# Kernel tuning notes

Measured on AMD Instinct MI355X. Metric: run time of the kernel, lower is better.

Reference implementation:

```python
import jax, jax.numpy as jnp
import numpy as np

SEQ_LEN = 720
PRED_LEN = 720
RANK = 16
CTX_DIM = 128
HID = 64
BATCH = 256


def setup_inputs() -> dict:
    key = jax.random.key(0)
    ks = jax.random.split(key, 8)
    x = jax.random.normal(ks[0], (BATCH, SEQ_LEN, 1), dtype=jnp.float32)
    ctx = jax.random.normal(ks[1], (BATCH, CTX_DIM), dtype=jnp.float32)
    # Base weight, xavier-uniform init
    limit = np.sqrt(6.0 / (PRED_LEN + SEQ_LEN)).astype(np.float32)
    W = jax.random.uniform(ks[2], (PRED_LEN, SEQ_LEN), dtype=jnp.float32,
                           minval=-limit, maxval=limit)
    # hyper MLP: Linear(ctx_dim, 64) -> ReLU -> Linear(64, rank*(seq+pred))
    out_dim = RANK * (SEQ_LEN + PRED_LEN)
    b1_lim = 1.0 / np.sqrt(CTX_DIM)
    W1 = jax.random.uniform(ks[3], (HID, CTX_DIM), dtype=jnp.float32, minval=-b1_lim, maxval=b1_lim)
    b1 = jax.random.uniform(ks[4], (HID,), dtype=jnp.float32, minval=-b1_lim, maxval=b1_lim)
    b2_lim = 1.0 / np.sqrt(HID)
    W2 = jax.random.uniform(ks[5], (out_dim, HID), dtype=jnp.float32, minval=-b2_lim, maxval=b2_lim)
    b2 = jax.random.uniform(ks[6], (out_dim,), dtype=jnp.float32, minval=-b2_lim, maxval=b2_lim)
    return {"x": x, "ctx": ctx, "W": W, "W1": W1, "b1": b1, "W2": W2, "b2": b2}


def reference(x, ctx, W, W1, b1, W2, b2):
    B = x.shape[0]
    # hyper MLP
    h = jax.nn.relu(ctx @ W1.T + b1) @ W2.T + b2  # (B, rank*(seq+pred))
    A_delta = h[:, : RANK * PRED_LEN].reshape(B, PRED_LEN, RANK)
    B_delta = h[:, RANK * PRED_LEN:].reshape(B, RANK, SEQ_LEN)
    # per-sample effective weight (materialized, as in the original)
    W_eff = W[None] + jnp.einsum('bpr,brs->bps', A_delta, B_delta)  # (B, pred, seq)
    y = jnp.einsum('bps,bs->bp', W_eff, x[..., 0])  # (B, pred)
    return (y[..., None], W_eff)
```

## Files before the change

kernel.cpp:

```cpp
#include <hip/hip_runtime.h>

#define SEQ  720
#define PRED 720
#define RANK 16
#define CTXD 128
#define HID  64
#define BATCH 256
#define ODIM  (RANK * (SEQ + PRED))
#define ASIZE (RANK * PRED)

#define PT 16
#define ST 256

typedef float v4f __attribute__((ext_vector_type(4)));

#define FMA4(ci, av, bv)                 \
    ci.x = fmaf(av, bv.x, ci.x);         \
    ci.y = fmaf(av, bv.y, ci.y);         \
    ci.z = fmaf(av, bv.z, ci.z);         \
    ci.w = fmaf(av, bv.w, ci.w);

__global__ __launch_bounds__(64) void k_hidden(const float* __restrict__ ctx,
                                               const float* __restrict__ W1,
                                               const float* __restrict__ b1,
                                               float* __restrict__ hid)
{
    __shared__ alignas(16) float cl[CTXD];
    int b = blockIdx.x, k = threadIdx.x;
    cl[k]      = ctx[b * CTXD + k];
    cl[k + 64] = ctx[b * CTXD + k + 64];
    __syncthreads();
    float acc = b1[k];
    const float* wr = W1 + k * CTXD;
#pragma unroll
    for (int c = 0; c < CTXD; c += 4) {
        float4 w  = *(const float4*)(wr + c);
        float4 xv = *(const float4*)(cl + c);
        acc = fmaf(w.x, xv.x, acc);
        acc = fmaf(w.y, xv.y, acc);
        acc = fmaf(w.z, xv.z, acc);
        acc = fmaf(w.w, xv.w, acc);
    }
    hid[b * HID + k] = fmaxf(acc, 0.0f);
}

__global__ __launch_bounds__(256) void k_hyper(const float* __restrict__ hid,
                                               const float* __restrict__ W2,
                                               const float* __restrict__ b2,
                                               float* __restrict__ h)
{
    int ot = blockIdx.x, bt = blockIdx.y;
    __shared__ alignas(16) float Hl[64 * 68];
    __shared__ alignas(16) float Wl[64 * 68];
    int tid = threadIdx.x;

    const float* hg = hid + (size_t)bt * 64 * HID;
    const float* wg = W2  + (size_t)ot * 64 * HID;
#pragma unroll
    for (int n = 0; n < 4; n++) {
        int g = tid * 4 + n * 1024;
        float4 hv = *(const float4*)(hg + g);
        float4 wv = *(const float4*)(wg + g);
        int row = g >> 6, colk = g & 63;
        *(float4*)&Hl[row * 68 + colk] = hv;
        *(float4*)&Wl[row * 68 + colk] = wv;
    }
    __syncthreads();

    int tx = tid & 15, ty = tid >> 4;
    float c[4][4];
#pragma unroll
    for (int j = 0; j < 4; j++) {
        float bv = b2[ot * 64 + j * 16 + tx];
        c[0][j] = bv; c[1][j] = bv; c[2][j] = bv; c[3][j] = bv;
    }
#pragma unroll
    for (int kc = 0; kc < HID; kc += 4) {
        float4 hv[4], wv[4];
#pragma unroll
        for (int i = 0; i < 4; i++) hv[i] = *(const float4*)&Hl[(ty * 4 + i) * 68 + kc];
#pragma unroll
        for (int j = 0; j < 4; j++) wv[j] = *(const float4*)&Wl[(j * 16 + tx) * 68 + kc];
#pragma unroll
        for (int i = 0; i < 4; i++)
#pragma unroll
            for (int j = 0; j < 4; j++) {
                c[i][j] = fmaf(hv[i].x, wv[j].x, c[i][j]);
                c[i][j] = fmaf(hv[i].y, wv[j].y, c[i][j]);
                c[i][j] = fmaf(hv[i].z, wv[j].z, c[i][j]);
                c[i][j] = fmaf(hv[i].w, wv[j].w, c[i][j]);
            }
    }
#pragma unroll
    for (int i = 0; i < 4; i++) {
        int b = bt * 64 + ty * 4 + i;
        float* hb = h + (size_t)b * ODIM + ot * 64;
#pragma unroll
        for (int j = 0; j < 4; j++)
            hb[j * 16 + tx] = c[i][j];
    }
}

__global__ __launch_bounds__(256) void k_y(const float* __restrict__ h,
                                           const float* __restrict__ W,
                                           const float* __restrict__ x,
                                           float* __restrict__ y)
{
    const int b = blockIdx.x, tid = threadIdx.x;
    __shared__ alignas(16) float xs[SEQ];
    __shared__ float red[256];
    __shared__ float bxs[RANK];
    const float* hb = h + (size_t)b * ODIM;

    if (tid < SEQ / 4)
        *(float4*)&xs[tid * 4] = *(const float4*)(x + (size_t)b * SEQ + tid * 4);
    __syncthreads();

    {
        const int r = tid >> 4, c = tid & 15;
        const float* brow = hb + ASIZE + r * SEQ + c * 45;
        float part = 0.0f;
#pragma unroll
        for (int i = 0; i < 45; i++) part = fmaf(brow[i], xs[c * 45 + i], part);
        red[tid] = part;
    }
    __syncthreads();
    if (tid < RANK) {
        float s = 0.0f;
#pragma unroll
        for (int j = 0; j < 16; j++) s += red[tid * 16 + j];
        bxs[tid] = s;
    }
    __syncthreads();

    for (int p = tid; p < PRED; p += 256) {
        const float* wr = W + (size_t)p * SEQ;
        float acc = 0.0f;
#pragma unroll 4
        for (int c4 = 0; c4 < SEQ; c4 += 4) {
            float4 wv = *(const float4*)(wr + c4);
            acc = fmaf(wv.x, xs[c4],     acc);
            acc = fmaf(wv.y, xs[c4 + 1], acc);
            acc = fmaf(wv.z, xs[c4 + 2], acc);
            acc = fmaf(wv.w, xs[c4 + 3], acc);
        }
        const float* ar = hb + p * RANK;
#pragma unroll
        for (int r = 0; r < RANK; r++) acc = fmaf(ar[r], bxs[r], acc);
        y[(size_t)b * PRED + p] = acc;
    }
}

__global__ __launch_bounds__(256, 4) void k_weff(const float* __restrict__ h,
                                                 const float* __restrict__ W,
                                                 float* __restrict__ weff)
{
    const int st = blockIdx.x, pt = blockIdx.y, b = blockIdx.z;
    const int s0 = st * ST, p0 = pt * PT;
    __shared__ alignas(16) float Al[PT * RANK];
    __shared__ alignas(16) float Bl[RANK][ST];
    const int tid = threadIdx.x;
    const float* hb = h + (size_t)b * ODIM;

    if (tid < (PT * RANK / 4))
        *(float4*)&Al[tid * 4] = *(const float4*)(hb + p0 * RANK + tid * 4);

    {
        const int r = tid >> 4, c4 = tid & 15;
        const float* brow = hb + ASIZE + r * SEQ;
#pragma unroll
        for (int q = 0; q < 4; q++) {
            int col = q * 64 + c4 * 4;
            float4 v = make_float4(0.f, 0.f, 0.f, 0.f);
            if (s0 + col < SEQ) v = *(const float4*)(brow + s0 + col);
            *(float4*)&Bl[r][col] = v;
        }
    }
    __syncthreads();

    const int wave = tid >> 6, lane = tid & 63;
    const int s = s0 + lane * 4;
    const bool sv = (s < SEQ);
    const int pbase = p0 + wave * 4;

    float4 c[4];
#pragma unroll
    for (int k = 0; k < 4; k++) c[k] = make_float4(0.f, 0.f, 0.f, 0.f);

#pragma unroll
    for (int rc = 0; rc < RANK; rc += 4) {
        float4 bb[4];
#pragma unroll
        for (int j = 0; j < 4; j++) bb[j] = *(const float4*)&Bl[rc + j][lane * 4];
#pragma unroll
        for (int k = 0; k < 4; k++) {
            float4 a = *(const float4*)&Al[(wave * 4 + k) * RANK + rc];
            FMA4(c[k], a.x, bb[0]);
            FMA4(c[k], a.y, bb[1]);
            FMA4(c[k], a.z, bb[2]);
            FMA4(c[k], a.w, bb[3]);
        }
    }

    if (sv) {
        float* wb = weff + (size_t)b * ((size_t)PRED * SEQ) + s;
        v4f e[4];
#pragma unroll
        for (int k = 0; k < 4; k++) {
            float4 wv = *(const float4*)(W + (size_t)(pbase + k) * SEQ + s);
            e[k].x = wv.x + c[k].x;
            e[k].y = wv.y + c[k].y;
            e[k].z = wv.z + c[k].z;
            e[k].w = wv.w + c[k].w;
        }
#pragma unroll
        for (int k = 0; k < 4; k++)
            __builtin_nontemporal_store(e[k], (v4f*)(wb + (size_t)(pbase + k) * SEQ));
    }
}

extern "C" void kernel_launch(void* const* d_in, const int* in_sizes, int n_in,
                              void* d_out, int out_size, void* d_ws, size_t ws_size,
                              hipStream_t stream)
{
    const float* x   = (const float*)d_in[0];
    const float* ctx = (const float*)d_in[1];
    const float* W   = (const float*)d_in[2];
    const float* W1  = (const float*)d_in[3];
    const float* b1  = (const float*)d_in[4];
    const float* W2  = (const float*)d_in[5];
    const float* b2  = (const float*)d_in[6];

    float* out  = (float*)d_out;
    float* yout = out;
    float* weff = out + (size_t)BATCH * PRED;

    float* hid = (float*)d_ws;
    float* h   = hid + (size_t)BATCH * HID;

    k_hidden<<<dim3(BATCH), dim3(64), 0, stream>>>(ctx, W1, b1, hid);
    k_hyper<<<dim3(ODIM / 64, BATCH / 64), dim3(256), 0, stream>>>(hid, W2, b2, h);
    k_y<<<dim3(BATCH), dim3(256), 0, stream>>>(h, W, x, yout);
    k_weff<<<dim3(SEQ / ST + 1, PRED / PT, BATCH), dim3(256), 0, stream>>>(h, W, weff);
}
```

Before: 646.0 us.

## Restructure W_eff kernel to keep B columns in registers and loop over all rows

Each k_weff block now covers one 256-column strip of a sample's full 720x720 output instead of a 16-row tile. The block stages the whole A factor in shared memory, and each thread holds its 16 B-factor float4 columns in registers. Each wave then streams 180 rows, fusing the W load, the rank-16 FMA and a nontemporal store. This removes repeated A/B staging and the many small blocks, but drops the grid to 768 blocks, uses about 46KB of LDS and more registers (occupancy 3), and puts shared-memory A reads inside the per-row loop.

```diff
diff --git a/kernel.cpp b/kernel.cpp
--- a/kernel.cpp
+++ b/kernel.cpp
@@ -9,8 +9,8 @@
 #define ODIM  (RANK * (SEQ + PRED))
 #define ASIZE (RANK * PRED)
 
-#define PT 16
 #define ST 256
+#define RPWAVE (PRED / 4)
 
 typedef float v4f __attribute__((ext_vector_type(4)));
 
@@ -151,71 +151,55 @@
     }
 }
 
-__global__ __launch_bounds__(256, 4) void k_weff(const float* __restrict__ h,
+__global__ __launch_bounds__(256, 3) void k_weff(const float* __restrict__ h,
                                                  const float* __restrict__ W,
                                                  float* __restrict__ weff)
 {
-    const int st = blockIdx.x, pt = blockIdx.y, b = blockIdx.z;
-    const int s0 = st * ST, p0 = pt * PT;
-    __shared__ alignas(16) float Al[PT * RANK];
-    __shared__ alignas(16) float Bl[RANK][ST];
+    const int st = blockIdx.x, b = blockIdx.y;
+    const int s0 = st * ST;
+    __shared__ alignas(16) float Al[PRED * RANK];
     const int tid = threadIdx.x;
     const float* hb = h + (size_t)b * ODIM;
 
-    if (tid < (PT * RANK / 4))
-        *(float4*)&Al[tid * 4] = *(const float4*)(hb + p0 * RANK + tid * 4);
-
-    {
-        const int r = tid >> 4, c4 = tid & 15;
-        const float* brow = hb + ASIZE + r * SEQ;
-#pragma unroll
-        for (int q = 0; q < 4; q++) {
-            int col = q * 64 + c4 * 4;
-            float4 v = make_float4(0.f, 0.f, 0.f, 0.f);
-            if (s0 + col < SEQ) v = *(const float4*)(brow + s0 + col);
-            *(float4*)&Bl[r][col] = v;
-        }
-    }
-    __syncthreads();
+    for (int i = tid; i < ASIZE / 4; i += 256)
+        *(float4*)&Al[i * 4] = *(const float4*)(hb + i * 4);
 
     const int wave = tid >> 6, lane = tid & 63;
     const int s = s0 + lane * 4;
     const bool sv = (s < SEQ);
-    const int pbase = p0 + wave * 4;
-
-    float4 c[4];
-#pragma unroll
-    for (int k = 0; k < 4; k++) c[k] = make_float4(0.f, 0.f, 0.f, 0.f);
-
-#pragma unroll
-    for (int rc = 0; rc < RANK; rc += 4) {
-        float4 bb[4];
-#pragma unroll
-        for (int j = 0; j < 4; j++) bb[j] = *(const float4*)&Bl[rc + j][lane * 4];
-#pragma unroll
-        for (int k = 0; k < 4; k++) {
-            float4 a = *(const float4*)&Al[(wave * 4 + k) * RANK + rc];
-            FMA4(c[k], a.x, bb[0]);
-            FMA4(c[k], a.y, bb[1]);
-            FMA4(c[k], a.z, bb[2]);
-            FMA4(c[k], a.w, bb[3]);
+    const int sc = sv ? s : (SEQ - 4);
+
+    float4 Bv[RANK];
+#pragma unroll
+    for (int r = 0; r < RANK; r++) {
+        float4 v = make_float4(0.f, 0.f, 0.f, 0.f);
+        if (sv) v = *(const float4*)(hb + ASIZE + r * SEQ + s);
+        Bv[r] = v;
+    }
+    __syncthreads();
+
+    const int p0 = wave * RPWAVE;
+    const float* wrow = W + (size_t)p0 * SEQ + sc;
+    const float* arow = Al + p0 * RANK;
+    float* orow = weff + (size_t)b * ((size_t)PRED * SEQ) + (size_t)p0 * SEQ + s;
+
+#pragma unroll 2
+    for (int i = 0; i < RPWAVE; ++i) {
+        float4 wv = *(const float4*)wrow;
+        v4f e;
+        e.x = wv.x; e.y = wv.y; e.z = wv.z; e.w = wv.w;
+#pragma unroll
+        for (int rc = 0; rc < RANK; rc += 4) {
+            float4 a = *(const float4*)(arow + rc);
+            FMA4(e, a.x, Bv[rc]);
+            FMA4(e, a.y, Bv[rc + 1]);
+            FMA4(e, a.z, Bv[rc + 2]);
+            FMA4(e, a.w, Bv[rc + 3]);
         }
-    }
-
-    if (sv) {
-        float* wb = weff + (size_t)b * ((size_t)PRED * SEQ) + s;
-        v4f e[4];
-#pragma unroll
-        for (int k = 0; k < 4; k++) {
-            float4 wv = *(const float4*)(W + (size_t)(pbase + k) * SEQ + s);
-            e[k].x = wv.x + c[k].x;
-            e[k].y = wv.y + c[k].y;
-            e[k].z = wv.z + c[k].z;
-            e[k].w = wv.w + c[k].w;
-        }
-#pragma unroll
-        for (int k = 0; k < 4; k++)
-            __builtin_nontemporal_store(e[k], (v4f*)(wb + (size_t)(pbase + k) * SEQ));
+        if (sv) __builtin_nontemporal_store(e, (v4f*)orow);
+        wrow += SEQ;
+        arow += RANK;
+        orow += SEQ;
     }
 }
 
@@ -241,5 +225,5 @@
     k_hidden<<<dim3(BATCH), dim3(64), 0, stream>>>(ctx, W1, b1, hid);
     k_hyper<<<dim3(ODIM / 64, BATCH / 64), dim3(256), 0, stream>>>(hid, W2, b2, h);
     k_y<<<dim3(BATCH), dim3(256), 0, stream>>>(h, W, x, yout);
-    k_weff<<<dim3(SEQ / ST + 1, PRED / PT, BATCH), dim3(256), 0, stream>>>(h, W, weff);
-}
+    k_weff<<<dim3(3, BATCH), dim3(256), 0, stream>>>(h, W, weff);
+}
```

New measurement: 649.0 us. No clear change (+0.5%).
